# Performance work log

Measured on AMD Instinct MI355X. Metric: run time of the kernel, lower is better.

## Reference

```python
import jax, jax.numpy as jnp
import numpy as np

H = 256          # hidden_dim
NH = 4           # num_heads
HD = H // NH     # head_dim = 64
EPS = 1e-5


def _ln(x, g, b):
    m = jnp.mean(x, axis=-1, keepdims=True)
    v = jnp.mean(jnp.square(x - m), axis=-1, keepdims=True)
    return (x - m) * jax.lax.rsqrt(v + EPS) * g + b


def _mha1(q_in, kv_in, in_proj_w, in_proj_b, out_w, out_b):
    # Single-query / single-key multihead attention (seq_len == 1 on both sides).
    # q_in, kv_in: [B, H]
    Wq, Wk, Wv = jnp.split(in_proj_w, 3, axis=0)   # each [H, H]
    bq, bk, bv = jnp.split(in_proj_b, 3, axis=0)
    B = q_in.shape[0]
    q = (q_in @ Wq.T + bq).reshape(B, NH, HD)
    k = (kv_in @ Wk.T + bk).reshape(B, NH, HD)
    v = (kv_in @ Wv.T + bv).reshape(B, NH, HD)
    scores = jnp.sum(q * k, axis=-1, keepdims=True) / jnp.sqrt(jnp.float32(HD))  # [B,NH,1]
    w = jax.nn.softmax(scores, axis=-1)  # softmax over 1 key -> all ones
    out = (w * v).reshape(B, H)
    return out @ out_w.T + out_b


def setup_inputs() -> dict:
    key = jax.random.key(0)
    ks = jax.random.split(key, 16)
    B, BIO, TXT, NC = 65536, 32, 768, 2
    s = lambda n: 1.0 / np.sqrt(n)
    return {
        "bio": jax.random.normal(ks[0], (B, BIO), jnp.float32),
        "text": jax.random.normal(ks[1], (B, TXT), jnp.float32),
        "bio_w": jax.random.normal(ks[2], (H, BIO), jnp.float32) * s(BIO),
        "bio_b": jnp.zeros((H,), jnp.float32),
        "text_w": jax.random.normal(ks[3], (H, TXT), jnp.float32) * s(TXT),
        "text_b": jnp.zeros((H,), jnp.float32),
        "ln_bio_g": jnp.ones((H,), jnp.float32),
        "ln_bio_b": jnp.zeros((H,), jnp.float32),
        "ln_text_g": jnp.ones((H,), jnp.float32),
        "ln_text_b": jnp.zeros((H,), jnp.float32),
        "in_proj_w": jax.random.normal(ks[4], (3 * H, H), jnp.float32) * s(H),
        "in_proj_b": jnp.zeros((3 * H,), jnp.float32),
        "out_w": jax.random.normal(ks[5], (H, H), jnp.float32) * s(H),
        "out_b": jnp.zeros((H,), jnp.float32),
        "cls1_w": jax.random.normal(ks[6], (H, 2 * H), jnp.float32) * s(2 * H),
        "cls1_b": jnp.zeros((H,), jnp.float32),
        "cls_ln_g": jnp.ones((H,), jnp.float32),
        "cls_ln_b": jnp.zeros((H,), jnp.float32),
        "cls2_w": jax.random.normal(ks[7], (NC, H), jnp.float32) * s(H),
        "cls2_b": jnp.zeros((NC,), jnp.float32),
    }


def reference(bio, text, bio_w, bio_b, text_w, text_b, ln_bio_g, ln_bio_b,
              ln_text_g, ln_text_b, in_proj_w, in_proj_b, out_w, out_b,
              cls1_w, cls1_b, cls_ln_g, cls_ln_b, cls2_w, cls2_b):
    b = _ln(bio @ bio_w.T + bio_b, ln_bio_g, ln_bio_b)      # [B, H]
    t = _ln(text @ text_w.T + text_b, ln_text_g, ln_text_b)  # [B, H]
    attn_bio = _mha1(b, t, in_proj_w, in_proj_b, out_w, out_b)
    attn_text = _mha1(t, b, in_proj_w, in_proj_b, out_w, out_b)
    fused = jnp.concatenate([attn_bio, attn_text], axis=-1)  # [B, 2H]
    h = jax.nn.relu(_ln(fused @ cls1_w.T + cls1_b, cls_ln_g, cls_ln_b))
    return h @ cls2_w.T + cls2_b
```

## Files before the change

kernel.cpp:

```cpp
#include <hip/hip_runtime.h>

typedef __attribute__((ext_vector_type(4))) float f4;
typedef __attribute__((ext_vector_type(2))) float f2;
typedef __attribute__((ext_vector_type(8))) short s8;

#define EPS 1e-5f

__device__ __forceinline__ unsigned short f2bf(float f) {
    union { float f; unsigned u; } v; v.f = f;
    unsigned u = v.u;
    return (unsigned short)((u + 0x7fffu + ((u >> 16) & 1u)) >> 16);
}
__device__ __forceinline__ unsigned pack2(float a, float b) {
    return (unsigned)f2bf(a) | ((unsigned)f2bf(b) << 16);
}

__device__ __forceinline__ unsigned cvt_pk2(float a, float b) {
    unsigned r;
    asm("v_cvt_pk_bf16_f32 %0, %1, %2" : "=v"(r) : "v"(a), "v"(b));
    return r;
}
__device__ __forceinline__ unsigned short cvt1(float a) {
    return (unsigned short)cvt_pk2(a, a);
}
__device__ __forceinline__ s8 pack8(f4 a, f4 b) {
    union { s8 v; unsigned u[4]; } r;
    r.u[0] = cvt_pk2(a[0], a[1]); r.u[1] = cvt_pk2(a[2], a[3]);
    r.u[2] = cvt_pk2(b[0], b[1]); r.u[3] = cvt_pk2(b[2], b[3]);
    return r.v;
}

__global__ __launch_bounds__(256) void k_prep1(const float* __restrict__ text_w,
                                               const float* __restrict__ bio_w,
                                               const float* __restrict__ out_w,
                                               const float* __restrict__ in_proj_w,
                                               const float* __restrict__ in_proj_b,
                                               const float* __restrict__ out_b,
                                               unsigned short* __restrict__ twFL,
                                               unsigned short* __restrict__ bwFL,
                                               float* __restrict__ A,
                                               float* __restrict__ cvec) {
    int b = blockIdx.x, t = threadIdx.x;
    if (b < 96) {
        int idx = b * 256 + t;
        int ksg = idx >> 10;
        int rem = idx & 1023;
        int ct = rem >> 6, lane = rem & 63;
        int n  = ct * 16 + (lane & 15);
        int k0 = ksg * 32 + ((lane >> 4) << 3);
        const float* src = &text_w[n * 768 + k0];
        f4 a = *(const f4*)src, c = *(const f4*)(src + 4);
        unsigned* dst = (unsigned*)&twFL[idx * 8];
        dst[0] = pack2(a[0], a[1]); dst[1] = pack2(a[2], a[3]);
        dst[2] = pack2(c[0], c[1]); dst[3] = pack2(c[2], c[3]);
    } else if (b < 100) {
        int idx = (b - 96) * 256 + t;
        int ct = idx >> 6, lane = idx & 63;
        int n  = ct * 16 + (lane & 15);
        int k0 = (lane >> 4) << 3;
        const float* src = &bio_w[n * 32 + k0];
        f4 a = *(const f4*)src, c = *(const f4*)(src + 4);
        unsigned* dst = (unsigned*)&bwFL[idx * 8];
        dst[0] = pack2(a[0], a[1]); dst[1] = pack2(a[2], a[3]);
        dst[2] = pack2(c[0], c[1]); dst[3] = pack2(c[2], c[3]);
    } else {
        __shared__ float srow[256];
        __shared__ float red[256];
        int i = b - 100, j = t;
        srow[j] = out_w[i * 256 + j];
        __syncthreads();
        float acc = 0.f;
#pragma unroll 16
        for (int k = 0; k < 256; k++)
            acc = fmaf(srow[k], in_proj_w[(512 + k) * 256 + j], acc);
        A[i * 256 + j] = acc;
        red[j] = srow[j] * in_proj_b[512 + j];
        __syncthreads();
        for (int s = 128; s > 0; s >>= 1) {
            if (j < s) red[j] += red[j + s];
            __syncthreads();
        }
        if (j == 0) cvec[i] = red[0] + out_b[i];
    }
}

__global__ __launch_bounds__(256) void k_prep_PQ(const float* __restrict__ cls1_w,
                                                 const float* __restrict__ cls1_b,
                                                 const float* __restrict__ A,
                                                 const float* __restrict__ cvec,
                                                 const float* __restrict__ ln_text_g,
                                                 const float* __restrict__ ln_text_b,
                                                 const float* __restrict__ ln_bio_g,
                                                 const float* __restrict__ ln_bio_b,
                                                 unsigned short* __restrict__ pqFL,
                                                 float* __restrict__ dvec) {
    __shared__ float w1[256], w2[256], red[256];
    int i = blockIdx.x, j = threadIdx.x;
    w1[j] = cls1_w[i * 512 + j];
    w2[j] = cls1_w[i * 512 + 256 + j];
    __syncthreads();
    float rp = 0.f, rq = 0.f;
#pragma unroll 8
    for (int k = 0; k < 256; k++) {
        float a = A[k * 256 + j];
        rp = fmaf(w1[k], a, rp);
        rq = fmaf(w2[k], a, rq);
    }
    int ct   = i >> 4;
    int lane = (i & 15) | (((j >> 3) & 3) << 4);
    int jj   = j & 7;
    int ks1  = j >> 5;
    pqFL[(((ks1     ) * 16 + ct) * 64 + lane) * 8 + jj] = f2bf(rp * ln_text_g[j]);
    pqFL[(((ks1 + 8 ) * 16 + ct) * 64 + lane) * 8 + jj] = f2bf(rq * ln_bio_g[j]);
    red[j] = rp * ln_text_b[j] + rq * ln_bio_b[j] + (w1[j] + w2[j]) * cvec[j];
    __syncthreads();
    for (int s = 128; s > 0; s >>= 1) {
        if (j < s) red[j] += red[j + s];
        __syncthreads();
    }
    if (j == 0) dvec[i] = red[0] + cls1_b[i];
}

__global__ __launch_bounds__(512, 4) void k_main(
    const float* __restrict__ bio, const float* __restrict__ text,
    const float* __restrict__ bio_b, const float* __restrict__ text_b,
    const float* __restrict__ cls_ln_g, const float* __restrict__ cls_ln_b,
    const float* __restrict__ cls2_w, const float* __restrict__ cls2_b,
    const unsigned short* __restrict__ twFL, const unsigned short* __restrict__ bwFL,
    const unsigned short* __restrict__ pqFL, const float* __restrict__ dvec,
    float* __restrict__ out)
{
    __shared__ __align__(16) unsigned short s_n[64][520];
    __shared__ __align__(16) float s_red[64][6][2];

    const int tid  = threadIdx.x;
    const int wv   = tid >> 6;
    const int cs   = wv & 3;
    const int rh   = wv >> 2;
    const int lane = tid & 63;
    const int q    = lane >> 4;
    const int lr   = lane & 15;
    const int R0   = blockIdx.x * 64;

    f4 acc[2][4];
    float s1[2][4], s2[2][4], m_[2][4], iv_[2][4];

    f4 bioA[2], bioB[2];
#pragma unroll
    for (int rt = 0; rt < 2; rt++) {
        const float* p = &bio[(size_t)(R0 + rh * 32 + rt * 16 + lr) * 32 + q * 8];
        bioA[rt] = *(const f4*)p;
        bioB[rt] = *(const f4*)(p + 4);
    }
    s8 bfrb[4];
#pragma unroll
    for (int c = 0; c < 4; c++)
        bfrb[c] = *(const s8*)&bwFL[((cs * 4 + c) * 64 + lane) * 8];

#pragma unroll
    for (int rt = 0; rt < 2; rt++)
#pragma unroll
        for (int c = 0; c < 4; c++) acc[rt][c] = (f4){0.f, 0.f, 0.f, 0.f};
#pragma unroll
    for (int rt = 0; rt < 2; rt++) {
        s8 af = pack8(bioA[rt], bioB[rt]);
#pragma unroll
        for (int c = 0; c < 4; c++)
            acc[rt][c] = __builtin_amdgcn_mfma_f32_16x16x32_bf16(af, bfrb[c], acc[rt][c], 0, 0, 0);
    }
#pragma unroll
    for (int rt = 0; rt < 2; rt++)
#pragma unroll
        for (int r = 0; r < 4; r++) { s1[rt][r] = 0.f; s2[rt][r] = 0.f; }
#pragma unroll
    for (int rt = 0; rt < 2; rt++)
#pragma unroll
        for (int c = 0; c < 4; c++) {
            float bb = bio_b[cs * 64 + c * 16 + lr];
#pragma unroll
            for (int r = 0; r < 4; r++) {
                float x = acc[rt][c][r] + bb;
                acc[rt][c][r] = x;
                s1[rt][r] += x; s2[rt][r] += x * x;
            }
        }
#pragma unroll
    for (int off = 1; off < 16; off <<= 1)
#pragma unroll
        for (int rt = 0; rt < 2; rt++)
#pragma unroll
            for (int r = 0; r < 4; r++) {
                s1[rt][r] += __shfl_xor(s1[rt][r], off, 64);
                s2[rt][r] += __shfl_xor(s2[rt][r], off, 64);
            }
    if (lr == 0)
#pragma unroll
        for (int rt = 0; rt < 2; rt++)
#pragma unroll
            for (int r = 0; r < 4; r++) {
                int row = rh * 32 + rt * 16 + q * 4 + r;
                f2 v; v[0] = s1[rt][r]; v[1] = s2[rt][r];
                *(f2*)&s_red[row][cs][0] = v;
            }
    __syncthreads();
#pragma unroll
    for (int rt = 0; rt < 2; rt++)
#pragma unroll
        for (int r = 0; r < 4; r++) {
            int row = rh * 32 + rt * 16 + q * 4 + r;
            f4 v0 = *(const f4*)&s_red[row][0][0];
            f4 v1 = *(const f4*)&s_red[row][2][0];
            float t1 = v0[0] + v0[2] + v1[0] + v1[2];
            float t2 = v0[1] + v0[3] + v1[1] + v1[3];
            float mm = t1 * (1.f / 256.f);
            float vv = t2 * (1.f / 256.f) - mm * mm;
            m_[rt][r]  = mm;
            iv_[rt][r] = rsqrtf(vv + EPS);
        }
#pragma unroll
    for (int rt = 0; rt < 2; rt++)
#pragma unroll
        for (int c = 0; c < 4; c++) {
            int col = cs * 64 + c * 16 + lr;
#pragma unroll
            for (int r = 0; r < 4; r++)
                s_n[rh * 32 + rt * 16 + q * 4 + r][256 + col] =
                    cvt1((acc[rt][c][r] - m_[rt][r]) * iv_[rt][r]);
        }

#pragma unroll
    for (int rt = 0; rt < 2; rt++)
#pragma unroll
        for (int c = 0; c < 4; c++) acc[rt][c] = (f4){0.f, 0.f, 0.f, 0.f};

    const float* tp0 = text + (size_t)(R0 + rh * 32 + lr) * 768 + q * 8;
    const float* tp1 = tp0 + 16 * 768;
    const unsigned short* wb = twFL + (cs * 256 + lane) * 8;

#pragma unroll 4
    for (int ks = 0; ks < 24; ks++) {
        s8 bfr[4];
#pragma unroll
        for (int c = 0; c < 4; c++)
            bfr[c] = *(const s8*)&wb[(ks * 16 + c) * 512];
        f4 a0 = *(const f4*)(tp0 + ks * 32);
        f4 a1 = *(const f4*)(tp0 + ks * 32 + 4);
        f4 b0 = *(const f4*)(tp1 + ks * 32);
        f4 b1 = *(const f4*)(tp1 + ks * 32 + 4);
        s8 af0 = pack8(a0, a1);
        s8 af1 = pack8(b0, b1);
        __builtin_amdgcn_s_setprio(1);
#pragma unroll
        for (int c = 0; c < 4; c++)
            acc[0][c] = __builtin_amdgcn_mfma_f32_16x16x32_bf16(af0, bfr[c], acc[0][c], 0, 0, 0);
#pragma unroll
        for (int c = 0; c < 4; c++)
            acc[1][c] = __builtin_amdgcn_mfma_f32_16x16x32_bf16(af1, bfr[c], acc[1][c], 0, 0, 0);
        __builtin_amdgcn_s_setprio(0);
    }

#pragma unroll
    for (int rt = 0; rt < 2; rt++)
#pragma unroll
        for (int r = 0; r < 4; r++) { s1[rt][r] = 0.f; s2[rt][r] = 0.f; }
#pragma unroll
    for (int rt = 0; rt < 2; rt++)
#pragma unroll
        for (int c = 0; c < 4; c++) {
            float bb = text_b[cs * 64 + c * 16 + lr];
#pragma unroll
            for (int r = 0; r < 4; r++) {
                float x = acc[rt][c][r] + bb;
                acc[rt][c][r] = x;
                s1[rt][r] += x; s2[rt][r] += x * x;
            }
        }
#pragma unroll
    for (int off = 1; off < 16; off <<= 1)
#pragma unroll
        for (int rt = 0; rt < 2; rt++)
#pragma unroll
            for (int r = 0; r < 4; r++) {
                s1[rt][r] += __shfl_xor(s1[rt][r], off, 64);
                s2[rt][r] += __shfl_xor(s2[rt][r], off, 64);
            }
    __syncthreads();
    if (lr == 0)
#pragma unroll
        for (int rt = 0; rt < 2; rt++)
#pragma unroll
            for (int r = 0; r < 4; r++) {
                int row = rh * 32 + rt * 16 + q * 4 + r;
                f2 v; v[0] = s1[rt][r]; v[1] = s2[rt][r];
                *(f2*)&s_red[row][cs][0] = v;
            }
    __syncthreads();
#pragma unroll
    for (int rt = 0; rt < 2; rt++)
#pragma unroll
        for (int r = 0; r < 4; r++) {
            int row = rh * 32 + rt * 16 + q * 4 + r;
            f4 v0 = *(const f4*)&s_red[row][0][0];
            f4 v1 = *(const f4*)&s_red[row][2][0];
            float t1 = v0[0] + v0[2] + v1[0] + v1[2];
            float t2 = v0[1] + v0[3] + v1[1] + v1[3];
            float mm = t1 * (1.f / 256.f);
            float vv = t2 * (1.f / 256.f) - mm * mm;
            m_[rt][r]  = mm;
            iv_[rt][r] = rsqrtf(vv + EPS);
        }
#pragma unroll
    for (int rt = 0; rt < 2; rt++)
#pragma unroll
        for (int c = 0; c < 4; c++) {
            int col = cs * 64 + c * 16 + lr;
#pragma unroll
            for (int r = 0; r < 4; r++)
                s_n[rh * 32 + rt * 16 + q * 4 + r][col] =
                    cvt1((acc[rt][c][r] - m_[rt][r]) * iv_[rt][r]);
        }
    __syncthreads();

#pragma unroll
    for (int rt = 0; rt < 2; rt++)
#pragma unroll
        for (int c = 0; c < 4; c++) {
            float dv = dvec[cs * 64 + c * 16 + lr];
            acc[rt][c] = (f4){dv, dv, dv, dv};
        }
    const unsigned short* pb = pqFL + (cs * 256 + lane) * 8;
#pragma unroll 4
    for (int ks = 0; ks < 16; ks++) {
        s8 bfr[4];
#pragma unroll
        for (int c = 0; c < 4; c++)
            bfr[c] = *(const s8*)&pb[(ks * 16 + c) * 512];
        s8 af0 = *(const s8*)&s_n[rh * 32 + lr][ks * 32 + q * 8];
        s8 af1 = *(const s8*)&s_n[rh * 32 + 16 + lr][ks * 32 + q * 8];
        __builtin_amdgcn_s_setprio(1);
#pragma unroll
        for (int c = 0; c < 4; c++)
            acc[0][c] = __builtin_amdgcn_mfma_f32_16x16x32_bf16(af0, bfr[c], acc[0][c], 0, 0, 0);
#pragma unroll
        for (int c = 0; c < 4; c++)
            acc[1][c] = __builtin_amdgcn_mfma_f32_16x16x32_bf16(af1, bfr[c], acc[1][c], 0, 0, 0);
        __builtin_amdgcn_s_setprio(0);
    }

#pragma unroll
    for (int rt = 0; rt < 2; rt++)
#pragma unroll
        for (int r = 0; r < 4; r++) { s1[rt][r] = 0.f; s2[rt][r] = 0.f; }
#pragma unroll
    for (int rt = 0; rt < 2; rt++)
#pragma unroll
        for (int c = 0; c < 4; c++)
#pragma unroll
            for (int r = 0; r < 4; r++) {
                float x = acc[rt][c][r];
                s1[rt][r] += x; s2[rt][r] += x * x;
            }
#pragma unroll
    for (int off = 1; off < 16; off <<= 1)
#pragma unroll
        for (int rt = 0; rt < 2; rt++)
#pragma unroll
            for (int r = 0; r < 4; r++) {
                s1[rt][r] += __shfl_xor(s1[rt][r], off, 64);
                s2[rt][r] += __shfl_xor(s2[rt][r], off, 64);
            }
    __syncthreads();
    if (lr == 0)
#pragma unroll
        for (int rt = 0; rt < 2; rt++)
#pragma unroll
            for (int r = 0; r < 4; r++) {
                int row = rh * 32 + rt * 16 + q * 4 + r;
                f2 v; v[0] = s1[rt][r]; v[1] = s2[rt][r];
                *(f2*)&s_red[row][cs][0] = v;
            }
    __syncthreads();
#pragma unroll
    for (int rt = 0; rt < 2; rt++)
#pragma unroll
        for (int r = 0; r < 4; r++) {
            int row = rh * 32 + rt * 16 + q * 4 + r;
            f4 v0 = *(const f4*)&s_red[row][0][0];
            f4 v1 = *(const f4*)&s_red[row][2][0];
            float t1 = v0[0] + v0[2] + v1[0] + v1[2];
            float t2 = v0[1] + v0[3] + v1[1] + v1[3];
            float mm = t1 * (1.f / 256.f);
            float vv = t2 * (1.f / 256.f) - mm * mm;
            m_[rt][r]  = mm;
            iv_[rt][r] = rsqrtf(vv + EPS);
        }
    float po0[2][4], po1[2][4];
#pragma unroll
    for (int rt = 0; rt < 2; rt++)
#pragma unroll
        for (int r = 0; r < 4; r++) { po0[rt][r] = 0.f; po1[rt][r] = 0.f; }
#pragma unroll
    for (int rt = 0; rt < 2; rt++)
#pragma unroll
        for (int c = 0; c < 4; c++) {
            int col = cs * 64 + c * 16 + lr;
            float gg = cls_ln_g[col], bb = cls_ln_b[col];
            float c0 = cls2_w[col],   c1 = cls2_w[256 + col];
#pragma unroll
            for (int r = 0; r < 4; r++) {
                float h = fmaxf((acc[rt][c][r] - m_[rt][r]) * iv_[rt][r] * gg + bb, 0.f);
                po0[rt][r] = fmaf(h, c0, po0[rt][r]);
                po1[rt][r] = fmaf(h, c1, po1[rt][r]);
            }
        }
#pragma unroll
    for (int off = 1; off < 16; off <<= 1)
#pragma unroll
        for (int rt = 0; rt < 2; rt++)
#pragma unroll
            for (int r = 0; r < 4; r++) {
                po0[rt][r] += __shfl_xor(po0[rt][r], off, 64);
                po1[rt][r] += __shfl_xor(po1[rt][r], off, 64);
            }
    __syncthreads();
    if (lr == 0)
#pragma unroll
        for (int rt = 0; rt < 2; rt++)
#pragma unroll
            for (int r = 0; r < 4; r++) {
                int row = rh * 32 + rt * 16 + q * 4 + r;
                f2 v; v[0] = po0[rt][r]; v[1] = po1[rt][r];
                *(f2*)&s_red[row][cs][0] = v;
            }
    __syncthreads();
    if (tid < 64) {
        int row = tid;
        f4 a = *(const f4*)&s_red[row][0][0];
        f4 b = *(const f4*)&s_red[row][2][0];
        f2 o;
        o[0] = a[0] + a[2] + b[0] + b[2] + cls2_b[0];
        o[1] = a[1] + a[3] + b[1] + b[3] + cls2_b[1];
        *(f2*)&out[(size_t)(R0 + row) * 2] = o;
    }
}

extern "C" void kernel_launch(void* const* d_in, const int* in_sizes, int n_in,
                              void* d_out, int out_size, void* d_ws, size_t ws_size,
                              hipStream_t stream) {
    const float* bio       = (const float*)d_in[0];
    const float* text      = (const float*)d_in[1];
    const float* bio_w     = (const float*)d_in[2];
    const float* bio_b     = (const float*)d_in[3];
    const float* text_w    = (const float*)d_in[4];
    const float* text_b    = (const float*)d_in[5];
    const float* ln_bio_g  = (const float*)d_in[6];
    const float* ln_bio_b  = (const float*)d_in[7];
    const float* ln_text_g = (const float*)d_in[8];
    const float* ln_text_b = (const float*)d_in[9];
    const float* in_proj_w = (const float*)d_in[10];
    const float* in_proj_b = (const float*)d_in[11];
    const float* out_w     = (const float*)d_in[12];
    const float* out_b     = (const float*)d_in[13];
    const float* cls1_w    = (const float*)d_in[14];
    const float* cls1_b    = (const float*)d_in[15];
    const float* cls_ln_g  = (const float*)d_in[16];
    const float* cls_ln_b  = (const float*)d_in[17];
    const float* cls2_w    = (const float*)d_in[18];
    const float* cls2_b    = (const float*)d_in[19];
    float* out = (float*)d_out;

    float* ws   = (float*)d_ws;
    float* A    = ws;
    float* cvec = ws + 65536;
    float* dvec = ws + 65792;
    unsigned short* us   = (unsigned short*)(ws + 66048);
    unsigned short* twFL = us;
    unsigned short* bwFL = us + 196608;
    unsigned short* pqFL = us + 204800;

    k_prep1  <<<356, 256, 0, stream>>>(text_w, bio_w, out_w, in_proj_w, in_proj_b, out_b,
                                       twFL, bwFL, A, cvec);
    k_prep_PQ<<<256, 256, 0, stream>>>(cls1_w, cls1_b, A, cvec,
                                       ln_text_g, ln_text_b, ln_bio_g, ln_bio_b,
                                       pqFL, dvec);

    int nrows = in_sizes[0] / 32;
    k_main<<<nrows / 64, 512, 0, stream>>>(bio, text, bio_b, text_b,
                                           cls_ln_g, cls_ln_b, cls2_w, cls2_b,
                                           twFL, bwFL, pqFL, dvec, out);
}
```

Baseline: 444.6 us.

## Stage text tiles through LDS with async double-buffered global-to-LDS loads

The text GEMM now streams 64x96 fp32 chunks of the text input into a swizzled, double-buffered LDS region using global_load_lds, prefetching the next chunk while MFMAs run on the current one. Weight fragments for the text GEMM and the projection GEMM are register double-buffered, and the text and bio phases are reordered so text runs first, reusing the s_n buffer as staging space. The goal is to hide the latency of the dominant 768-wide text read behind compute, at the cost of a barrier per chunk, extra registers, and the removal of the setprio hints.

```diff
diff --git a/kernel.cpp b/kernel.cpp
--- a/kernel.cpp
+++ b/kernel.cpp
@@ -28,6 +28,21 @@
     r.u[0] = cvt_pk2(a[0], a[1]); r.u[1] = cvt_pk2(a[2], a[3]);
     r.u[2] = cvt_pk2(b[0], b[1]); r.u[3] = cvt_pk2(b[2], b[3]);
     return r.v;
+}
+
+#if defined(__has_builtin)
+#if __has_builtin(__builtin_amdgcn_global_load_lds)
+#define HAVE_GLLDS 1
+#endif
+#endif
+__device__ __forceinline__ void gl_lds16(const float* g, unsigned short* l) {
+#ifdef HAVE_GLLDS
+    __builtin_amdgcn_global_load_lds(
+        (const __attribute__((address_space(1))) unsigned int*)g,
+        (__attribute__((address_space(3))) unsigned int*)l, 16, 0, 0);
+#else
+    *(f4*)l = *(const f4*)g;
+#endif
 }
 
 __global__ __launch_bounds__(256) void k_prep1(const float* __restrict__ text_w,
@@ -142,8 +157,83 @@
     const int lr   = lane & 15;
     const int R0   = blockIdx.x * 64;
 
+    unsigned short* sx = (unsigned short*)s_n;
+    const int SXU = 12288;
+
     f4 acc[2][4];
     float s1[2][4], s2[2][4], m_[2][4], iv_[2][4];
+
+    int sfofs[3], sdofs[3];
+#pragma unroll
+    for (int i = 0; i < 3; i++) {
+        int idx = i * 512 + tid;
+        int row = idx / 24;
+        int j   = idx - row * 24;
+        sfofs[i] = (R0 + row) * 768 + ((j ^ (row & 7)) << 2);
+        sdofs[i] = idx * 8;
+    }
+    int offB[2][2];
+#pragma unroll
+    for (int rt = 0; rt < 2; rt++) {
+        int row = rh * 32 + rt * 16 + lr;
+        int sw  = (row & 7) << 4;
+        offB[rt][0] = (row * 384 + ((q * 32) ^ sw)) >> 1;
+        offB[rt][1] = (row * 384 + (((q * 32) + 16) ^ sw)) >> 1;
+    }
+
+#pragma unroll
+    for (int i = 0; i < 3; i++)
+        gl_lds16(text + sfofs[i], sx + sdofs[i]);
+
+    const unsigned short* wb = twFL + (cs * 256 + lane) * 8;
+    s8 wc[4], wn[4];
+#pragma unroll
+    for (int c = 0; c < 4; c++) wc[c] = *(const s8*)&wb[c * 512];
+#pragma unroll
+    for (int c = 0; c < 4; c++) wn[c] = wc[c];
+
+#pragma unroll
+    for (int rt = 0; rt < 2; rt++)
+#pragma unroll
+        for (int c = 0; c < 4; c++) acc[rt][c] = (f4){0.f, 0.f, 0.f, 0.f};
+
+    __syncthreads();
+
+    for (int ch = 0; ch < 8; ch++) {
+        const int buf = ch & 1;
+        if (ch < 7) {
+            const float* src = text + (ch + 1) * 96;
+            unsigned short* dst = sx + (buf ^ 1) * SXU;
+#pragma unroll
+            for (int i = 0; i < 3; i++)
+                gl_lds16(src + sfofs[i], dst + sdofs[i]);
+        }
+        const unsigned short* sb = sx + buf * SXU;
+#pragma unroll
+        for (int ks = 0; ks < 3; ks++) {
+            int kk = ch * 3 + ks;
+            if (kk < 23) {
+#pragma unroll
+                for (int c = 0; c < 4; c++)
+                    wn[c] = *(const s8*)&wb[((kk + 1) * 16 + c) * 512];
+            }
+            f4 lo0 = *(const f4*)&sb[offB[0][0] + ks * 64];
+            f4 hi0 = *(const f4*)&sb[offB[0][1] + ks * 64];
+            f4 lo1 = *(const f4*)&sb[offB[1][0] + ks * 64];
+            f4 hi1 = *(const f4*)&sb[offB[1][1] + ks * 64];
+            s8 af0 = pack8(lo0, hi0);
+            s8 af1 = pack8(lo1, hi1);
+#pragma unroll
+            for (int c = 0; c < 4; c++)
+                acc[0][c] = __builtin_amdgcn_mfma_f32_16x16x32_bf16(af0, wc[c], acc[0][c], 0, 0, 0);
+#pragma unroll
+            for (int c = 0; c < 4; c++)
+                acc[1][c] = __builtin_amdgcn_mfma_f32_16x16x32_bf16(af1, wc[c], acc[1][c], 0, 0, 0);
+#pragma unroll
+            for (int c = 0; c < 4; c++) wc[c] = wn[c];
+        }
+        __syncthreads();
+    }
 
     f4 bioA[2], bioB[2];
 #pragma unroll
@@ -160,23 +250,12 @@
 #pragma unroll
     for (int rt = 0; rt < 2; rt++)
 #pragma unroll
-        for (int c = 0; c < 4; c++) acc[rt][c] = (f4){0.f, 0.f, 0.f, 0.f};
-#pragma unroll
-    for (int rt = 0; rt < 2; rt++) {
-        s8 af = pack8(bioA[rt], bioB[rt]);
-#pragma unroll
-        for (int c = 0; c < 4; c++)
-            acc[rt][c] = __builtin_amdgcn_mfma_f32_16x16x32_bf16(af, bfrb[c], acc[rt][c], 0, 0, 0);
-    }
-#pragma unroll
-    for (int rt = 0; rt < 2; rt++)
-#pragma unroll
         for (int r = 0; r < 4; r++) { s1[rt][r] = 0.f; s2[rt][r] = 0.f; }
 #pragma unroll
     for (int rt = 0; rt < 2; rt++)
 #pragma unroll
         for (int c = 0; c < 4; c++) {
-            float bb = bio_b[cs * 64 + c * 16 + lr];
+            float bb = text_b[cs * 64 + c * 16 + lr];
 #pragma unroll
             for (int r = 0; r < 4; r++) {
                 float x = acc[rt][c][r] + bb;
@@ -224,7 +303,7 @@
             int col = cs * 64 + c * 16 + lr;
 #pragma unroll
             for (int r = 0; r < 4; r++)
-                s_n[rh * 32 + rt * 16 + q * 4 + r][256 + col] =
+                s_n[rh * 32 + rt * 16 + q * 4 + r][col] =
                     cvt1((acc[rt][c][r] - m_[rt][r]) * iv_[rt][r]);
         }
 
@@ -232,33 +311,13 @@
     for (int rt = 0; rt < 2; rt++)
 #pragma unroll
         for (int c = 0; c < 4; c++) acc[rt][c] = (f4){0.f, 0.f, 0.f, 0.f};
-
-    const float* tp0 = text + (size_t)(R0 + rh * 32 + lr) * 768 + q * 8;
-    const float* tp1 = tp0 + 16 * 768;
-    const unsigned short* wb = twFL + (cs * 256 + lane) * 8;
-
-#pragma unroll 4
-    for (int ks = 0; ks < 24; ks++) {
-        s8 bfr[4];
+#pragma unroll
+    for (int rt = 0; rt < 2; rt++) {
+        s8 af = pack8(bioA[rt], bioB[rt]);
 #pragma unroll
         for (int c = 0; c < 4; c++)
-            bfr[c] = *(const s8*)&wb[(ks * 16 + c) * 512];
-        f4 a0 = *(const f4*)(tp0 + ks * 32);
-        f4 a1 = *(const f4*)(tp0 + ks * 32 + 4);
-        f4 b0 = *(const f4*)(tp1 + ks * 32);
-        f4 b1 = *(const f4*)(tp1 + ks * 32 + 4);
-        s8 af0 = pack8(a0, a1);
-        s8 af1 = pack8(b0, b1);
-        __builtin_amdgcn_s_setprio(1);
-#pragma unroll
-        for (int c = 0; c < 4; c++)
-            acc[0][c] = __builtin_amdgcn_mfma_f32_16x16x32_bf16(af0, bfr[c], acc[0][c], 0, 0, 0);
-#pragma unroll
-        for (int c = 0; c < 4; c++)
-            acc[1][c] = __builtin_amdgcn_mfma_f32_16x16x32_bf16(af1, bfr[c], acc[1][c], 0, 0, 0);
-        __builtin_amdgcn_s_setprio(0);
-    }
-
+            acc[rt][c] = __builtin_amdgcn_mfma_f32_16x16x32_bf16(af, bfrb[c], acc[rt][c], 0, 0, 0);
+    }
 #pragma unroll
     for (int rt = 0; rt < 2; rt++)
 #pragma unroll
@@ -267,7 +326,7 @@
     for (int rt = 0; rt < 2; rt++)
 #pragma unroll
         for (int c = 0; c < 4; c++) {
-            float bb = text_b[cs * 64 + c * 16 + lr];
+            float bb = bio_b[cs * 64 + c * 16 + lr];
 #pragma unroll
             for (int r = 0; r < 4; r++) {
                 float x = acc[rt][c][r] + bb;
@@ -316,7 +375,7 @@
             int col = cs * 64 + c * 16 + lr;
 #pragma unroll
             for (int r = 0; r < 4; r++)
-                s_n[rh * 32 + rt * 16 + q * 4 + r][col] =
+                s_n[rh * 32 + rt * 16 + q * 4 + r][256 + col] =
                     cvt1((acc[rt][c][r] - m_[rt][r]) * iv_[rt][r]);
         }
     __syncthreads();
@@ -329,22 +388,28 @@
             acc[rt][c] = (f4){dv, dv, dv, dv};
         }
     const unsigned short* pb = pqFL + (cs * 256 + lane) * 8;
-#pragma unroll 4
+    s8 pc[4], pn[4];
+#pragma unroll
+    for (int c = 0; c < 4; c++) pc[c] = *(const s8*)&pb[c * 512];
+#pragma unroll
+    for (int c = 0; c < 4; c++) pn[c] = pc[c];
+#pragma unroll
     for (int ks = 0; ks < 16; ks++) {
-        s8 bfr[4];
-#pragma unroll
-        for (int c = 0; c < 4; c++)
-            bfr[c] = *(const s8*)&pb[(ks * 16 + c) * 512];
+        if (ks < 15) {
+#pragma unroll
+            for (int c = 0; c < 4; c++)
+                pn[c] = *(const s8*)&pb[((ks + 1) * 16 + c) * 512];
+        }
         s8 af0 = *(const s8*)&s_n[rh * 32 + lr][ks * 32 + q * 8];
         s8 af1 = *(const s8*)&s_n[rh * 32 + 16 + lr][ks * 32 + q * 8];
-        __builtin_amdgcn_s_setprio(1);
 #pragma unroll
         for (int c = 0; c < 4; c++)
-            acc[0][c] = __builtin_amdgcn_mfma_f32_16x16x32_bf16(af0, bfr[c], acc[0][c], 0, 0, 0);
+            acc[0][c] = __builtin_amdgcn_mfma_f32_16x16x32_bf16(af0, pc[c], acc[0][c], 0, 0, 0);
 #pragma unroll
         for (int c = 0; c < 4; c++)
-            acc[1][c] = __builtin_amdgcn_mfma_f32_16x16x32_bf16(af1, bfr[c], acc[1][c], 0, 0, 0);
-        __builtin_amdgcn_s_setprio(0);
+            acc[1][c] = __builtin_amdgcn_mfma_f32_16x16x32_bf16(af1, pc[c], acc[1][c], 0, 0, 0);
+#pragma unroll
+        for (int c = 0; c < 4; c++) pc[c] = pn[c];
     }
 
 #pragma unroll
@@ -369,7 +434,6 @@
                 s1[rt][r] += __shfl_xor(s1[rt][r], off, 64);
                 s2[rt][r] += __shfl_xor(s2[rt][r], off, 64);
             }
-    __syncthreads();
     if (lr == 0)
 #pragma unroll
         for (int rt = 0; rt < 2; rt++)
```

New measurement: 381.0 us. 1.17x faster.
